# Kernel optimization log

Hardware: AMD Instinct MI355X
Metric: run time of the kernel (lower is better)

## Reference

```python
import jax, jax.numpy as jnp
import numpy as np

B, N, M, ASN, P = 4096, 8, 16, 101, 3


def setup_inputs() -> dict:
    key = jax.random.key(0)
    k1, k2 = jax.random.split(key)
    X = jax.random.normal(k1, (B, N), dtype=jnp.float32)
    mu = 0.5 * jnp.ones((1, N, M, 1), dtype=jnp.float32)
    sigma = jnp.ones((1, N, M, 1), dtype=jnp.float32)
    delta_sig = 0.1 * jnp.ones((1, N, M, 1), dtype=jnp.float32)
    weights = jax.random.uniform(k2, (M, P), dtype=jnp.float32)
    bias = jnp.zeros((1, P), dtype=jnp.float32)
    alpha = jnp.linspace(0.0, 1.0, ASN, dtype=jnp.float32).reshape(1, 1, 1, -1)
    return {"X": X, "mu": mu, "sigma": sigma, "delta_sig": delta_sig,
            "weights": weights, "bias": bias, "alpha": alpha}


def reference(X, mu, sigma, delta_sig, weights, bias, alpha):
    # GT2_MF: sigma' = sigma + delta_sig/2, delta = delta_sig/2
    sig = sigma + delta_sig / 2
    delta = delta_sig / 2
    xe = X[:, :, None, None]                      # [B, N, 1, 1]
    one_m_a = 1.0 - alpha                         # [1, 1, 1, asn]
    lower = jnp.exp(-0.5 * ((xe - mu) / (sig + delta * one_m_a)) ** 2)  # [B,N,M,asn]
    upper = jnp.exp(-0.5 * ((xe - mu) / (sig - delta * one_m_a)) ** 2)
    f_up = jnp.prod(upper, axis=1)                # [B, M, asn]
    f_lo = jnp.prod(lower, axis=1)
    # Nie-Tan defuzzification
    f_sum = f_up + f_lo                           # [B, M, asn]
    num = jnp.einsum('bma,mp->bap', f_sum, weights)          # [B, asn, P]
    den = jnp.sum(f_sum, axis=1)[:, :, None]                 # [B, asn, 1]
    y_alpha = num / den                                      # [B, asn, P]
    a = alpha.reshape(1, -1, 1)
    y = jnp.sum(y_alpha * a, axis=1) / jnp.sum(alpha)        # [B, P]
    return y + bias
```

## Files before the change

### kernel.cpp

```cpp
#include <hip/hip_runtime.h>
#include <hip/hip_bf16.h>


constexpr int B = 4096, N = 8, M = 16, ASN = 101, P = 3;
constexpr float LOG2E = 1.4426950408889634f;

__global__ void build_ctab(const float* __restrict__ sigma,
                           const float* __restrict__ delta_sig,
                           const float* __restrict__ alpha,
                           float2* __restrict__ ctab) {
    int idx = blockIdx.x * blockDim.x + threadIdx.x;
    if (idx >= N * M * ASN) return;
    int a  = idx % ASN;
    int nm = idx / ASN;
    float dl  = delta_sig[nm] * 0.5f;
    float sg  = sigma[nm] + dl;
    float oma = 1.0f - alpha[a];
    float dlo = sg + dl * oma;
    float dup = sg - dl * oma;
    float cl = (-0.5f * LOG2E) / (dlo * dlo);
    float cu = (-0.5f * LOG2E) / (dup * dup);
    ctab[idx] = make_float2(cl, cu);
}

__global__ __launch_bounds__(128) void gt2rbf_main(
    const float*  __restrict__ X,
    const float*  __restrict__ mu,
    const float*  __restrict__ weights,
    const float*  __restrict__ bias,
    const float*  __restrict__ alpha,
    const float2* __restrict__ ctab,
    float* __restrict__ out)
{
    __shared__ float dsq[N * M];
    __shared__ float red[2][4];

    const int b = blockIdx.x;
    const int t = threadIdx.x;

    if (t < N * M) {
        int n = t >> 4;
        float d = X[b * N + n] - mu[t];
        dsq[t] = d * d;
    }
    __syncthreads();

    float c0 = 0.f, c1 = 0.f, c2 = 0.f, av = 0.f;
    if (t < ASN) {
        av = alpha[t];
        float num0 = 0.f, num1 = 0.f, num2 = 0.f, den = 0.f;
        #pragma unroll
        for (int m = 0; m < M; ++m) {
            float slo = 0.f, sup = 0.f;
            #pragma unroll
            for (int n = 0; n < N; ++n) {
                float q  = dsq[n * M + m];
                float2 c = ctab[(n * M + m) * ASN + t];
                slo = fmaf(q, c.x, slo);
                sup = fmaf(q, c.y, sup);
            }
            float f = exp2f(sup) + exp2f(slo);
            num0 = fmaf(f, weights[m * P + 0], num0);
            num1 = fmaf(f, weights[m * P + 1], num1);
            num2 = fmaf(f, weights[m * P + 2], num2);
            den += f;
        }
        float s = av / den;
        c0 = num0 * s; c1 = num1 * s; c2 = num2 * s;
    }

    #pragma unroll
    for (int off = 32; off > 0; off >>= 1) {
        c0 += __shfl_down(c0, off);
        c1 += __shfl_down(c1, off);
        c2 += __shfl_down(c2, off);
        av += __shfl_down(av, off);
    }
    const int wave = t >> 6;
    if ((t & 63) == 0) {
        red[wave][0] = c0; red[wave][1] = c1; red[wave][2] = c2; red[wave][3] = av;
    }
    __syncthreads();
    if (t == 0) {
        float asum = red[0][3] + red[1][3];
        float inv  = 1.0f / asum;
        out[b * P + 0] = (red[0][0] + red[1][0]) * inv + bias[0];
        out[b * P + 1] = (red[0][1] + red[1][1]) * inv + bias[1];
        out[b * P + 2] = (red[0][2] + red[1][2]) * inv + bias[2];
    }
}

extern "C" void kernel_launch(void* const* d_in, const int* in_sizes, int n_in,
                              void* d_out, int out_size, void* d_ws, size_t ws_size,
                              hipStream_t stream) {
    const float* X         = (const float*)d_in[0];
    const float* mu        = (const float*)d_in[1];
    const float* sigma     = (const float*)d_in[2];
    const float* delta_sig = (const float*)d_in[3];
    const float* weights   = (const float*)d_in[4];
    const float* bias      = (const float*)d_in[5];
    const float* alpha     = (const float*)d_in[6];
    float* out = (float*)d_out;

    float2* ctab = (float2*)d_ws;

    int tab = N * M * ASN;
    build_ctab<<<(tab + 255) / 256, 256, 0, stream>>>(sigma, delta_sig, alpha, ctab);
    gt2rbf_main<<<B, 128, 0, stream>>>(X, mu, weights, bias, alpha, ctab, out);
}
```

Baseline: 100.4 us.

## Process four batch rows per block and expand squared distance into precomputed coefficients

```diff
diff --git a/kernel.cpp b/kernel.cpp
--- a/kernel.cpp
+++ b/kernel.cpp
@@ -3,90 +3,158 @@
 
 
 constexpr int B = 4096, N = 8, M = 16, ASN = 101, P = 3;
+constexpr int KB = 4;
+constexpr int NBLK = B / KB;
 constexpr float LOG2E = 1.4426950408889634f;
 
-__global__ void build_ctab(const float* __restrict__ sigma,
+__global__ void build_ctab(const float* __restrict__ mu,
+                           const float* __restrict__ sigma,
                            const float* __restrict__ delta_sig,
                            const float* __restrict__ alpha,
-                           float2* __restrict__ ctab) {
+                           float4* __restrict__ c4,
+                           float2* __restrict__ c3) {
     int idx = blockIdx.x * blockDim.x + threadIdx.x;
-    if (idx >= N * M * ASN) return;
-    int a  = idx % ASN;
-    int nm = idx / ASN;
-    float dl  = delta_sig[nm] * 0.5f;
-    float sg  = sigma[nm] + dl;
-    float oma = 1.0f - alpha[a];
-    float dlo = sg + dl * oma;
-    float dup = sg - dl * oma;
-    float cl = (-0.5f * LOG2E) / (dlo * dlo);
-    float cu = (-0.5f * LOG2E) / (dup * dup);
-    ctab[idx] = make_float2(cl, cu);
+    constexpr int MNA = M * N * ASN;
+    if (idx < MNA) {
+        int a = idx % ASN;
+        int mn = idx / ASN;
+        int m = mn / N, n = mn % N;
+        int nm = n * M + m;
+        float dl = delta_sig[nm] * 0.5f;
+        float sg = sigma[nm] + dl;
+        float oma = 1.0f - alpha[a];
+        float dlo = sg + dl * oma;
+        float dup = sg - dl * oma;
+        float kl = (-0.5f * LOG2E) / (dlo * dlo);
+        float ku = (-0.5f * LOG2E) / (dup * dup);
+        float mv = mu[nm];
+        c4[idx] = make_float4(kl, -2.0f * mv * kl, ku, -2.0f * mv * ku);
+    } else if (idx < MNA + M * ASN) {
+        int j = idx - MNA;
+        int a = j % ASN, m = j / ASN;
+        float oma = 1.0f - alpha[a];
+        float sl = 0.f, su = 0.f;
+        for (int n = 0; n < N; ++n) {
+            int nm = n * M + m;
+            float dl = delta_sig[nm] * 0.5f;
+            float sg = sigma[nm] + dl;
+            float dlo = sg + dl * oma;
+            float dup = sg - dl * oma;
+            float kl = (-0.5f * LOG2E) / (dlo * dlo);
+            float ku = (-0.5f * LOG2E) / (dup * dup);
+            float mv = mu[nm];
+            sl = fmaf(mv * mv, kl, sl);
+            su = fmaf(mv * mv, ku, su);
+        }
+        c3[m * ASN + a] = make_float2(sl, su);
+    }
 }
 
 __global__ __launch_bounds__(128) void gt2rbf_main(
     const float*  __restrict__ X,
-    const float*  __restrict__ mu,
     const float*  __restrict__ weights,
     const float*  __restrict__ bias,
     const float*  __restrict__ alpha,
-    const float2* __restrict__ ctab,
+    const float4* __restrict__ c4,
+    const float2* __restrict__ c3,
     float* __restrict__ out)
 {
-    __shared__ float dsq[N * M];
-    __shared__ float red[2][4];
+    __shared__ float wl[M * P];
+    __shared__ float red[2][KB * P + 1];
 
-    const int b = blockIdx.x;
     const int t = threadIdx.x;
+    const int bg = blockIdx.x;
 
-    if (t < N * M) {
-        int n = t >> 4;
-        float d = X[b * N + n] - mu[t];
-        dsq[t] = d * d;
+    if (t < M * P) wl[t] = weights[t];
+
+    float xv[KB][N], x2[KB][N];
+    const float* Xb = X + bg * (KB * N);
+    #pragma unroll
+    for (int i = 0; i < KB; ++i)
+        #pragma unroll
+        for (int n = 0; n < N; ++n) {
+            float v = Xb[i * N + n];
+            xv[i][n] = v;
+            x2[i][n] = v * v;
+        }
+    __syncthreads();
+
+    float vals[KB * P + 1];
+    #pragma unroll
+    for (int k = 0; k < KB * P + 1; ++k) vals[k] = 0.f;
+
+    if (t < ASN) {
+        float av = alpha[t];
+        float num[KB][P], den[KB];
+        #pragma unroll
+        for (int i = 0; i < KB; ++i) {
+            den[i] = 0.f;
+            #pragma unroll
+            for (int p = 0; p < P; ++p) num[i][p] = 0.f;
+        }
+
+        #pragma unroll 2
+        for (int m = 0; m < M; ++m) {
+            float2 C = c3[m * ASN + t];
+            float slo[KB], sup[KB];
+            #pragma unroll
+            for (int i = 0; i < KB; ++i) { slo[i] = C.x; sup[i] = C.y; }
+
+            #pragma unroll
+            for (int n = 0; n < N; ++n) {
+                float4 c = c4[(m * N + n) * ASN + t];
+                #pragma unroll
+                for (int i = 0; i < KB; ++i) {
+                    slo[i] = fmaf(x2[i][n], c.x, fmaf(xv[i][n], c.y, slo[i]));
+                    sup[i] = fmaf(x2[i][n], c.z, fmaf(xv[i][n], c.w, sup[i]));
+                }
+            }
+
+            float w0 = wl[m * P + 0], w1 = wl[m * P + 1], w2 = wl[m * P + 2];
+            #pragma unroll
+            for (int i = 0; i < KB; ++i) {
+                float f = exp2f(slo[i]) + exp2f(sup[i]);
+                num[i][0] = fmaf(f, w0, num[i][0]);
+                num[i][1] = fmaf(f, w1, num[i][1]);
+                num[i][2] = fmaf(f, w2, num[i][2]);
+                den[i] += f;
+            }
+        }
+
+        #pragma unroll
+        for (int i = 0; i < KB; ++i) {
+            float s = av / den[i];
+            vals[i * P + 0] = num[i][0] * s;
+            vals[i * P + 1] = num[i][1] * s;
+            vals[i * P + 2] = num[i][2] * s;
+        }
+        vals[KB * P] = av;
+    }
+
+    #pragma unroll
+    for (int off = 32; off > 0; off >>= 1)
+        #pragma unroll
+        for (int k = 0; k < KB * P + 1; ++k)
+            vals[k] += __shfl_down(vals[k], off);
+
+    const int w = t >> 6;
+    if ((t & 63) == 0) {
+        #pragma unroll
+        for (int k = 0; k < KB * P + 1; ++k) red[w][k] = vals[k];
     }
     __syncthreads();
 
-    float c0 = 0.f, c1 = 0.f, c2 = 0.f, av = 0.f;
-    if (t < ASN) {
-        av = alpha[t];
-        float num0 = 0.f, num1 = 0.f, num2 = 0.f, den = 0.f;
+    if (t == 0) {
+        float asum = red[0][KB * P] + red[1][KB * P];
+        float inv = 1.0f / asum;
         #pragma unroll
-        for (int m = 0; m < M; ++m) {
-            float slo = 0.f, sup = 0.f;
+        for (int i = 0; i < KB; ++i) {
             #pragma unroll
-            for (int n = 0; n < N; ++n) {
-                float q  = dsq[n * M + m];
-                float2 c = ctab[(n * M + m) * ASN + t];
-                slo = fmaf(q, c.x, slo);
-                sup = fmaf(q, c.y, sup);
+            for (int p = 0; p < P; ++p) {
+                out[(bg * KB + i) * P + p] =
+                    (red[0][i * P + p] + red[1][i * P + p]) * inv + bias[p];
             }
-            float f = exp2f(sup) + exp2f(slo);
-            num0 = fmaf(f, weights[m * P + 0], num0);
-            num1 = fmaf(f, weights[m * P + 1], num1);
-            num2 = fmaf(f, weights[m * P + 2], num2);
-            den += f;
         }
-        float s = av / den;
-        c0 = num0 * s; c1 = num1 * s; c2 = num2 * s;
-    }
-
-    #pragma unroll
-    for (int off = 32; off > 0; off >>= 1) {
-        c0 += __shfl_down(c0, off);
-        c1 += __shfl_down(c1, off);
-        c2 += __shfl_down(c2, off);
-        av += __shfl_down(av, off);
-    }
-    const int wave = t >> 6;
-    if ((t & 63) == 0) {
-        red[wave][0] = c0; red[wave][1] = c1; red[wave][2] = c2; red[wave][3] = av;
-    }
-    __syncthreads();
-    if (t == 0) {
-        float asum = red[0][3] + red[1][3];
-        float inv  = 1.0f / asum;
-        out[b * P + 0] = (red[0][0] + red[1][0]) * inv + bias[0];
-        out[b * P + 1] = (red[0][1] + red[1][1]) * inv + bias[1];
-        out[b * P + 2] = (red[0][2] + red[1][2]) * inv + bias[2];
     }
 }
 
@@ -102,9 +170,11 @@
     const float* alpha     = (const float*)d_in[6];
     float* out = (float*)d_out;
 
-    float2* ctab = (float2*)d_ws;
+    constexpr int MNA = M * N * ASN;
+    float4* c4 = (float4*)d_ws;
+    float2* c3 = (float2*)((char*)d_ws + MNA * sizeof(float4));
 
-    int tab = N * M * ASN;
-    build_ctab<<<(tab + 255) / 256, 256, 0, stream>>>(sigma, delta_sig, alpha, ctab);
-    gt2rbf_main<<<B, 128, 0, stream>>>(X, mu, weights, bias, alpha, ctab, out);
+    constexpr int total = MNA + M * ASN;
+    build_ctab<<<(total + 255) / 256, 256, 0, stream>>>(mu, sigma, delta_sig, alpha, c4, c3);
+    gt2rbf_main<<<NBLK, 128, 0, stream>>>(X, weights, bias, alpha, c4, c3, out);
 }
```

Measured after the change: 86.23 us, median of 2. 14.1% less time.
